# Kernel optimization log

Hardware: AMD Instinct MI355X
Metric: run time of the kernel (lower is better)

## Reference

```python
import jax, jax.numpy as jnp
import numpy as np

D_MODEL = 1024
N_HEADS = 16
D_HEAD = D_MODEL // N_HEADS
ROPE_BASE = 10000.0


def _rotate_half(x):
    half = x.shape[-1] // 2
    x1, x2 = x[..., :half], x[..., half:]
    return jnp.concatenate([-x2, x1], axis=-1)


def _rope_cos_sin(seq_len, d_head, dtype):
    inv_freq = 1.0 / (ROPE_BASE ** (jnp.arange(0, d_head, 2, dtype=jnp.float32) / d_head))
    t = jnp.arange(seq_len, dtype=jnp.float32)
    freqs = jnp.outer(t, inv_freq)                       # [S, d_head/2]
    emb = jnp.concatenate([freqs, freqs], axis=-1)       # [S, d_head]
    return jnp.cos(emb).astype(dtype), jnp.sin(emb).astype(dtype)


def setup_inputs() -> dict:
    key = jax.random.key(0)
    k1, k2, k3 = jax.random.split(key, 3)
    B, S = 2, 2048
    x = jax.random.normal(k1, (B, S, D_MODEL), dtype=jnp.float32)
    # torch nn.Linear weight layout: [out_features, in_features], y = x @ W.T
    w_qkv = jax.random.normal(k2, (3 * D_MODEL, D_MODEL), dtype=jnp.float32) * (D_MODEL ** -0.5)
    w_out = jax.random.normal(k3, (D_MODEL, D_MODEL), dtype=jnp.float32) * (D_MODEL ** -0.5)
    return {"x": x, "w_qkv": w_qkv, "w_out": w_out}


def reference(x, w_qkv, w_out):
    B, S, _ = x.shape
    qkv = jnp.einsum('bsd,ed->bse', x, w_qkv)            # [B, S, 3*D]
    qkv = qkv.reshape(B, S, 3, N_HEADS, D_HEAD)
    qkv = jnp.transpose(qkv, (2, 0, 3, 1, 4))            # [3, B, H, S, Dh]
    q, k, v = qkv[0], qkv[1], qkv[2]

    cos, sin = _rope_cos_sin(S, D_HEAD, x.dtype)         # [S, Dh] each
    cos = cos[None, None]                                # [1, 1, S, Dh]
    sin = sin[None, None]
    q = q * cos + _rotate_half(q) * sin
    k = k * cos + _rotate_half(k) * sin

    scale = 1.0 / jnp.sqrt(jnp.array(D_HEAD, dtype=x.dtype))
    attn = jnp.einsum('bhqd,bhkd->bhqk', q, k) * scale   # [B, H, S, S]
    causal = jnp.tril(jnp.ones((S, S), dtype=bool))      # triu(diag=1) masked -> keep lower tri
    attn = jnp.where(causal[None, None], attn, jnp.finfo(x.dtype).min)
    attn = jax.nn.softmax(attn, axis=-1)

    out = jnp.einsum('bhqk,bhkd->bhqd', attn, v)         # [B, H, S, Dh]
    out = jnp.transpose(out, (0, 2, 1, 3)).reshape(B, S, D_MODEL)
    return jnp.einsum('bsd,ed->bse', out, w_out)         # out_proj
```

## Files before the change

### kernel.cpp

```cpp
#include <hip/hip_runtime.h>
#include <hip/hip_bf16.h>
#include <cmath>

#define DMODEL 1024
#define NH 16
#define DH 64
#define SEQ 2048
#define BATCH 2

typedef __attribute__((ext_vector_type(8))) short bf16x8;
typedef __attribute__((ext_vector_type(4))) float f32x4;
typedef __attribute__((ext_vector_type(8))) unsigned short u16x8;

__device__ __forceinline__ unsigned short f2bf(float f) {
    unsigned int u = __builtin_bit_cast(unsigned int, f);
    u += 0x7fffu + ((u >> 16) & 1u);
    return (unsigned short)(u >> 16);
}
__device__ __forceinline__ float exp2_fast(float x) {
    float r;
    asm("v_exp_f32 %0, %1" : "=v"(r) : "v"(x));
    return r;
}

__global__ __launch_bounds__(256)
void cast_all(const float* __restrict__ x, const float* __restrict__ wq,
              const float* __restrict__ wo, unsigned short* __restrict__ xb,
              unsigned short* __restrict__ wqb, unsigned short* __restrict__ wob)
{
    const int i = blockIdx.x * 256 + threadIdx.x;
    const float* src; unsigned short* dst; int off;
    if (i < 524288)      { src = x;  dst = xb;  off = i; }
    else if (i < 917504) { src = wq; dst = wqb; off = i - 524288; }
    else                 { src = wo; dst = wob; off = i - 917504; }
    const float4 a = *(const float4*)(src + (size_t)off * 8);
    const float4 b = *(const float4*)(src + (size_t)off * 8 + 4);
    u16x8 o;
    o[0] = f2bf(a.x); o[1] = f2bf(a.y); o[2] = f2bf(a.z); o[3] = f2bf(a.w);
    o[4] = f2bf(b.x); o[5] = f2bf(b.y); o[6] = f2bf(b.z); o[7] = f2bf(b.w);
    *(u16x8*)(dst + (size_t)off * 8) = o;
}

template<int BM, int EPI>
__global__ __launch_bounds__(256)
void gemm_bf16(const unsigned short* __restrict__ A,
               const unsigned short* __restrict__ B,
               float* __restrict__ oc, unsigned short* __restrict__ oq,
               unsigned short* __restrict__ ok, unsigned short* __restrict__ ovt,
               int M, int N)
{
    constexpr int K = 1024;
    constexpr int BK = 32;
    constexpr int NT = K / BK;
    constexpr int FM = BM / 32;
    __shared__ unsigned short As[2][BM * BK];
    __shared__ unsigned short Bs[2][128 * BK];

    const int t  = threadIdx.x;
    const int l  = t & 63;
    const int w  = t >> 6;
    const int g  = l >> 4;
    const int ln = l & 15;
    const int wr = w >> 1, wc = w & 1;
    const int m0 = blockIdx.y * BM;
    const int n0 = blockIdx.x * 128;

    auto stage = [&](int kt, int bufi) {
        #pragma unroll
        for (int i = 0; i < BM / 64; ++i) {
            const int n = i * 256 + t;
            const int r = n >> 2, slot = n & 3;
            const int kk = kt * BK + ((slot ^ ((r >> 1) & 3)) * 8);
            const unsigned short* ga = A + (size_t)(m0 + r) * K + kk;
            __builtin_amdgcn_global_load_lds(
                (const __attribute__((address_space(1))) unsigned int*)ga,
                (__attribute__((address_space(3))) unsigned int*)&As[bufi][n * 8], 16, 0, 0);
        }
        #pragma unroll
        for (int i = 0; i < 2; ++i) {
            const int n = i * 256 + t;
            const int r = n >> 2, slot = n & 3;
            const int kk = kt * BK + ((slot ^ ((r >> 1) & 3)) * 8);
            const unsigned short* gb = B + (size_t)(n0 + r) * K + kk;
            __builtin_amdgcn_global_load_lds(
                (const __attribute__((address_space(1))) unsigned int*)gb,
                (__attribute__((address_space(3))) unsigned int*)&Bs[bufi][n * 8], 16, 0, 0);
        }
    };

    f32x4 acc[FM][4];
    #pragma unroll
    for (int i = 0; i < FM; ++i)
        #pragma unroll
        for (int j = 0; j < 4; ++j) acc[i][j] = (f32x4){0.f, 0.f, 0.f, 0.f};

    const int swz = (g ^ ((ln >> 1) & 3)) << 4;

    stage(0, 0);
    for (int kt = 0; kt < NT; ++kt) {
        __syncthreads();
        if (kt + 1 < NT) stage(kt + 1, (kt + 1) & 1);
        const char* as = (const char*)As[kt & 1];
        const char* bs = (const char*)Bs[kt & 1];
        bf16x8 af[FM], bfr[4];
        #pragma unroll
        for (int fm = 0; fm < FM; ++fm)
            af[fm] = *(const bf16x8*)(as + (wr * (BM / 2) + fm * 16 + ln) * 64 + swz);
        #pragma unroll
        for (int fn = 0; fn < 4; ++fn)
            bfr[fn] = *(const bf16x8*)(bs + (wc * 64 + fn * 16 + ln) * 64 + swz);
        #pragma unroll
        for (int fm = 0; fm < FM; ++fm)
            #pragma unroll
            for (int fn = 0; fn < 4; ++fn)
                acc[fm][fn] = __builtin_amdgcn_mfma_f32_16x16x32_bf16(
                    af[fm], bfr[fn], acc[fm][fn], 0, 0, 0);
    }

    const int rowbase = m0 + wr * (BM / 2);
    const int colbase = n0 + wc * 64;
    if (EPI == 1) {
        #pragma unroll
        for (int fm = 0; fm < FM; ++fm)
            #pragma unroll
            for (int fn = 0; fn < 4; ++fn)
                #pragma unroll
                for (int rr = 0; rr < 4; ++rr) {
                    const int row = rowbase + fm * 16 + g * 4 + rr;
                    oc[(size_t)row * N + colbase + fn * 16 + ln] = acc[fm][fn][rr];
                }
    } else {
        const int which = colbase >> 10;
        const int h = (colbase >> 6) & (NH - 1);
        if (which < 2) {
            unsigned short* dst = which == 0 ? oq : ok;
            const float scale = which == 0 ? 0.18033688011112042f : 1.f;
            const float cexp = -13.287712379549449f / 32.f;
            const float if0 = exp2f((float)ln * cexp);
            const float if1 = exp2f((float)(16 + ln) * cexp);
            #pragma unroll
            for (int fm = 0; fm < FM; ++fm)
                #pragma unroll
                for (int rr = 0; rr < 4; ++rr) {
                    const int row = rowbase + fm * 16 + g * 4 + rr;
                    const int b = row >> 11, s = row & (SEQ - 1);
                    float s0, c0, s1, c1;
                    __sincosf((float)s * if0, &s0, &c0);
                    __sincosf((float)s * if1, &s1, &c1);
                    const float x0 = acc[fm][0][rr], x1 = acc[fm][1][rr];
                    const float x2 = acc[fm][2][rr], x3 = acc[fm][3][rr];
                    const size_t base = (((size_t)b * NH + h) * SEQ + s) * DH;
                    dst[base + ln]      = f2bf((x0 * c0 - x2 * s0) * scale);
                    dst[base + 16 + ln] = f2bf((x1 * c1 - x3 * s1) * scale);
                    dst[base + 32 + ln] = f2bf((x2 * c0 + x0 * s0) * scale);
                    dst[base + 48 + ln] = f2bf((x3 * c1 + x1 * s1) * scale);
                }
        } else {
            #pragma unroll
            for (int fm = 0; fm < FM; ++fm)
                #pragma unroll
                for (int fn = 0; fn < 4; ++fn) {
                    const int row = rowbase + fm * 16 + g * 4;
                    const int b = row >> 11, s = row & (SEQ - 1);
                    const int d = fn * 16 + ln;
                    ushort4 pk;
                    pk.x = f2bf(acc[fm][fn][0]); pk.y = f2bf(acc[fm][fn][1]);
                    pk.z = f2bf(acc[fm][fn][2]); pk.w = f2bf(acc[fm][fn][3]);
                    *(ushort4*)&ovt[(((size_t)b * NH + h) * DH + d) * SEQ + s] = pk;
                }
        }
    }
}

__global__ __launch_bounds__(256)
void attn_mfma(const unsigned short* __restrict__ q,
               const unsigned short* __restrict__ k,
               const unsigned short* __restrict__ vt,
               unsigned short* __restrict__ ob)
{
    __shared__ unsigned short Ks[2][64 * 64];
    __shared__ unsigned short Vs[2][64 * 64];
    __shared__ unsigned short Ps[2][4][16 * 64];

    const int t  = threadIdx.x;
    const int l  = t & 63;
    const int w  = t >> 6;
    const int g  = l >> 4;
    const int ln = l & 15;
    const int pi = blockIdx.x;
    const int qtA = pi, qtB = 31 - pi;
    const int bh = blockIdx.y;
    const size_t bqk = (size_t)bh * SEQ * DH;
    const size_t bv  = (size_t)bh * DH * SEQ;

    bf16x8 qfA0, qfA1, qfB0, qfB1;
    {
        const unsigned short* qa = q + bqk + (size_t)(qtA * 64 + w * 16 + ln) * DH + g * 8;
        qfA0 = *(const bf16x8*)qa;  qfA1 = *(const bf16x8*)(qa + 32);
        const unsigned short* qb2 = q + bqk + (size_t)(qtB * 64 + w * 16 + ln) * DH + g * 8;
        qfB0 = *(const bf16x8*)qb2; qfB1 = *(const bf16x8*)(qb2 + 32);
    }

    f32x4 aoA[4], aoB[4];
    #pragma unroll
    for (int i = 0; i < 4; ++i) {
        aoA[i] = (f32x4){0.f, 0.f, 0.f, 0.f};
        aoB[i] = (f32x4){0.f, 0.f, 0.f, 0.f};
    }
    float lA = 0.f, lB = 0.f;

    auto stage = [&](int kt, int bufi) {
        #pragma unroll
        for (int rr = 0; rr < 2; ++rr) {
            const int id  = rr * 256 + t;
            const int row = id >> 3, sl = id & 7;
            const int slg = (sl ^ (row & 7)) * 8;
            const unsigned short* gk = k  + bqk + (size_t)(kt * 64 + row) * DH + slg;
            const unsigned short* gv = vt + bv  + (size_t)row * SEQ + kt * 64 + slg;
            __builtin_amdgcn_global_load_lds(
                (const __attribute__((address_space(1))) unsigned int*)gk,
                (__attribute__((address_space(3))) unsigned int*)&Ks[bufi][id * 8], 16, 0, 0);
            __builtin_amdgcn_global_load_lds(
                (const __attribute__((address_space(1))) unsigned int*)gv,
                (__attribute__((address_space(3))) unsigned int*)&Vs[bufi][id * 8], 16, 0, 0);
        }
    };

    auto softmax_tile = [&](f32x4* s, float& l_, char* pb) {
        const float M2 = 28.853900817779268f;
        float rs = 0.f;
        #pragma unroll
        for (int nb = 0; nb < 4; ++nb) {
            float e[4];
            #pragma unroll
            for (int r = 0; r < 4; ++r)
                e[r] = exp2_fast(s[nb][r] - M2);
            rs += (e[0] + e[1]) + (e[2] + e[3]);
            uint2 dw;
            dw.x = __builtin_amdgcn_perm(
                __builtin_bit_cast(unsigned int, e[1]),
                __builtin_bit_cast(unsigned int, e[0]), 0x07060302u);
            dw.y = __builtin_amdgcn_perm(
                __builtin_bit_cast(unsigned int, e[3]),
                __builtin_bit_cast(unsigned int, e[2]), 0x07060302u);
            *(uint2*)(pb + ((nb * 32 + g * 8) ^ ((ln & 7) << 4))) = dw;
        }
        rs += __shfl_xor(rs, 16);
        rs += __shfl_xor(rs, 32);
        l_ += rs;
    };

    char* pbA = (char*)&Ps[0][w][0] + ln * 128;
    char* pbB = (char*)&Ps[1][w][0] + ln * 128;

    stage(0, 0);
    for (int kt = 0; kt <= qtB; ++kt) {
        __syncthreads();
        if (kt < qtB) stage(kt + 1, (kt + 1) & 1);
        const bool actA = (kt <= qtA);
        const char* kb = (const char*)Ks[kt & 1];
        const char* vb = (const char*)Vs[kt & 1];

        f32x4 sA[4], sB[4];
        #pragma unroll
        for (int nb = 0; nb < 4; ++nb) {
            sA[nb] = (f32x4){0.f, 0.f, 0.f, 0.f};
            sB[nb] = (f32x4){0.f, 0.f, 0.f, 0.f};
        }
        __builtin_amdgcn_s_setprio(1);
        #pragma unroll
        for (int nb = 0; nb < 4; ++nb) {
            const int key = nb * 16 + ln;
            const char* kr = kb + key * 128;
            bf16x8 kf0 = *(const bf16x8*)(kr + ((g ^ (key & 7)) << 4));
            bf16x8 kf1 = *(const bf16x8*)(kr + (((g + 4) ^ (key & 7)) << 4));
            sB[nb] = __builtin_amdgcn_mfma_f32_16x16x32_bf16(kf0, qfB0, sB[nb], 0, 0, 0);
            sB[nb] = __builtin_amdgcn_mfma_f32_16x16x32_bf16(kf1, qfB1, sB[nb], 0, 0, 0);
            if (actA) {
                sA[nb] = __builtin_amdgcn_mfma_f32_16x16x32_bf16(kf0, qfA0, sA[nb], 0, 0, 0);
                sA[nb] = __builtin_amdgcn_mfma_f32_16x16x32_bf16(kf1, qfA1, sA[nb], 0, 0, 0);
            }
        }
        __builtin_amdgcn_s_setprio(0);

        if (kt == qtB) {
            #pragma unroll
            for (int nb = 0; nb < 4; ++nb)
                #pragma unroll
                for (int r = 0; r < 4; ++r)
                    if (nb * 16 + g * 4 + r > w * 16 + ln) sB[nb][r] = -INFINITY;
        }
        if (kt == qtA) {
            #pragma unroll
            for (int nb = 0; nb < 4; ++nb)
                #pragma unroll
                for (int r = 0; r < 4; ++r)
                    if (nb * 16 + g * 4 + r > w * 16 + ln) sA[nb][r] = -INFINITY;
        }

        softmax_tile(sB, lB, pbB);
        if (actA) softmax_tile(sA, lA, pbA);

        __builtin_amdgcn_s_setprio(1);
        #pragma unroll
        for (int ks = 0; ks < 2; ++ks) {
            bf16x8 pfB = *(const bf16x8*)(pbB + ((ks * 64 + g * 16) ^ ((ln & 7) << 4)));
            bf16x8 pfA;
            if (actA)
                pfA = *(const bf16x8*)(pbA + ((ks * 64 + g * 16) ^ ((ln & 7) << 4)));
            #pragma unroll
            for (int db = 0; db < 4; ++db) {
                const int d = db * 16 + ln;
                bf16x8 vf = *(const bf16x8*)(vb + d * 128 + (((ks * 4 + g) ^ (d & 7)) << 4));
                aoB[db] = __builtin_amdgcn_mfma_f32_16x16x32_bf16(pfB, vf, aoB[db], 0, 0, 0);
                if (actA)
                    aoA[db] = __builtin_amdgcn_mfma_f32_16x16x32_bf16(pfA, vf, aoA[db], 0, 0, 0);
            }
        }
        __builtin_amdgcn_s_setprio(0);
    }

    const int b = bh >> 4, h = bh & (NH - 1);
    const float invA = 1.f / lA, invB = 1.f / lB;
    #pragma unroll
    for (int r = 0; r < 4; ++r) {
        const float iA = __shfl(invA, g * 4 + r);
        const float iB = __shfl(invB, g * 4 + r);
        const size_t rowA = (size_t)(b * SEQ + qtA * 64 + w * 16 + g * 4 + r) * DMODEL + h * DH;
        const size_t rowB = (size_t)(b * SEQ + qtB * 64 + w * 16 + g * 4 + r) * DMODEL + h * DH;
        #pragma unroll
        for (int db = 0; db < 4; ++db) {
            ob[rowA + db * 16 + ln] = f2bf(aoA[db][r] * iA);
            ob[rowB + db * 16 + ln] = f2bf(aoB[db][r] * iB);
        }
    }
}

extern "C" void kernel_launch(void* const* d_in, const int* in_sizes, int n_in,
                              void* d_out, int out_size, void* d_ws, size_t ws_size,
                              hipStream_t stream)
{
    const float* x  = (const float*)d_in[0];
    const float* wq = (const float*)d_in[1];
    const float* wo = (const float*)d_in[2];
    float* out = (float*)d_out;

    const size_t NQ = (size_t)BATCH * NH * SEQ * DH;
    unsigned short* qb  = (unsigned short*)d_ws;
    unsigned short* kb  = qb + NQ;
    unsigned short* vtb = kb + NQ;
    unsigned short* ob  = vtb + NQ;
    unsigned short* xb  = ob + NQ;
    unsigned short* wqb = xb + NQ;
    unsigned short* wob = wqb + 3 * DMODEL * DMODEL;

    cast_all<<<4096, 256, 0, stream>>>(x, wq, wo, xb, wqb, wob);

    dim3 g1(3072 / 128, 4096 / 128);
    gemm_bf16<128, 0><<<g1, 256, 0, stream>>>(xb, wqb, nullptr, qb, kb, vtb, 4096, 3072);

    dim3 g2(16, BATCH * NH);
    attn_mfma<<<g2, 256, 0, stream>>>(qb, kb, vtb, ob);

    dim3 g3(1024 / 128, 4096 / 64);
    gemm_bf16<64, 1><<<g3, 256, 0, stream>>>(ob, wob, out, nullptr, nullptr, nullptr, 4096, 1024);
}
```

Baseline: 124.4 us.

## Keep softmax probabilities in registers by permuting key order in QK^T tiles

Reorders which keys each MFMA lane group computes in the QK^T step, so the output accumulator layout matches the A-operand layout needed for the PV MFMA. This lets the bf16 probabilities stay in registers instead of being written to and read back from an LDS staging buffer. The K/V LDS swizzle and causal mask indices are changed to match the new key permutation. The per-tile row-sum shuffles are moved out of the loop into a single reduction at the end. The index mapping is subtle, and any mismatch between the new swizzle and the permutation would give wrong results or LDS bank conflicts.

```diff
diff --git a/kernel.cpp b/kernel.cpp
--- a/kernel.cpp
+++ b/kernel.cpp
@@ -10,6 +10,7 @@
 
 typedef __attribute__((ext_vector_type(8))) short bf16x8;
 typedef __attribute__((ext_vector_type(4))) float f32x4;
+typedef __attribute__((ext_vector_type(4))) unsigned int u32x4;
 typedef __attribute__((ext_vector_type(8))) unsigned short u16x8;
 
 __device__ __forceinline__ unsigned short f2bf(float f) {
@@ -180,7 +181,6 @@
 {
     __shared__ unsigned short Ks[2][64 * 64];
     __shared__ unsigned short Vs[2][64 * 64];
-    __shared__ unsigned short Ps[2][4][16 * 64];
 
     const int t  = threadIdx.x;
     const int l  = t & 63;
@@ -214,7 +214,8 @@
         for (int rr = 0; rr < 2; ++rr) {
             const int id  = rr * 256 + t;
             const int row = id >> 3, sl = id & 7;
-            const int slg = (sl ^ (row & 7)) * 8;
+            const int sg  = (row & 3) | (((row >> 3) & 1) << 2);
+            const int slg = (sl ^ sg) * 8;
             const unsigned short* gk = k  + bqk + (size_t)(kt * 64 + row) * DH + slg;
             const unsigned short* gv = vt + bv  + (size_t)row * SEQ + kt * 64 + slg;
             __builtin_amdgcn_global_load_lds(
@@ -226,9 +227,16 @@
         }
     };
 
-    auto softmax_tile = [&](f32x4* s, float& l_, char* pb) {
+    const int rowoffK = ((ln >> 2) * 8 + (ln & 3)) * 128;
+    const int sK = (ln & 3) | (((ln >> 2) & 1) << 2);
+    const int slotK0 = ((g ^ sK) << 4);
+    const int slotK1 = (((g + 4) ^ sK) << 4);
+    const int sV = (ln & 3) | (((ln >> 3) & 1) << 2);
+
+    auto softmax_tile = [&](f32x4* s, float& l_, bf16x8* pf) {
         const float M2 = 28.853900817779268f;
         float rs = 0.f;
+        unsigned int dw[8];
         #pragma unroll
         for (int nb = 0; nb < 4; ++nb) {
             float e[4];
@@ -236,22 +244,17 @@
             for (int r = 0; r < 4; ++r)
                 e[r] = exp2_fast(s[nb][r] - M2);
             rs += (e[0] + e[1]) + (e[2] + e[3]);
-            uint2 dw;
-            dw.x = __builtin_amdgcn_perm(
+            dw[nb * 2] = __builtin_amdgcn_perm(
                 __builtin_bit_cast(unsigned int, e[1]),
                 __builtin_bit_cast(unsigned int, e[0]), 0x07060302u);
-            dw.y = __builtin_amdgcn_perm(
+            dw[nb * 2 + 1] = __builtin_amdgcn_perm(
                 __builtin_bit_cast(unsigned int, e[3]),
                 __builtin_bit_cast(unsigned int, e[2]), 0x07060302u);
-            *(uint2*)(pb + ((nb * 32 + g * 8) ^ ((ln & 7) << 4))) = dw;
-        }
-        rs += __shfl_xor(rs, 16);
-        rs += __shfl_xor(rs, 32);
+        }
         l_ += rs;
+        pf[0] = __builtin_bit_cast(bf16x8, (u32x4){dw[0], dw[1], dw[2], dw[3]});
+        pf[1] = __builtin_bit_cast(bf16x8, (u32x4){dw[4], dw[5], dw[6], dw[7]});
     };
-
-    char* pbA = (char*)&Ps[0][w][0] + ln * 128;
-    char* pbB = (char*)&Ps[1][w][0] + ln * 128;
 
     stage(0, 0);
     for (int kt = 0; kt <= qtB; ++kt) {
@@ -270,10 +273,9 @@
         __builtin_amdgcn_s_setprio(1);
         #pragma unroll
         for (int nb = 0; nb < 4; ++nb) {
-            const int key = nb * 16 + ln;
-            const char* kr = kb + key * 128;
-            bf16x8 kf0 = *(const bf16x8*)(kr + ((g ^ (key & 7)) << 4));
-            bf16x8 kf1 = *(const bf16x8*)(kr + (((g + 4) ^ (key & 7)) << 4));
+            const char* kr = kb + ((nb >> 1) * 32 + (nb & 1) * 4) * 128 + rowoffK;
+            bf16x8 kf0 = *(const bf16x8*)(kr + slotK0);
+            bf16x8 kf1 = *(const bf16x8*)(kr + slotK1);
             sB[nb] = __builtin_amdgcn_mfma_f32_16x16x32_bf16(kf0, qfB0, sB[nb], 0, 0, 0);
             sB[nb] = __builtin_amdgcn_mfma_f32_16x16x32_bf16(kf1, qfB1, sB[nb], 0, 0, 0);
             if (actA) {
@@ -288,38 +290,39 @@
             for (int nb = 0; nb < 4; ++nb)
                 #pragma unroll
                 for (int r = 0; r < 4; ++r)
-                    if (nb * 16 + g * 4 + r > w * 16 + ln) sB[nb][r] = -INFINITY;
+                    if ((nb >> 1) * 32 + g * 8 + (nb & 1) * 4 + r > w * 16 + ln)
+                        sB[nb][r] = -INFINITY;
         }
         if (kt == qtA) {
             #pragma unroll
             for (int nb = 0; nb < 4; ++nb)
                 #pragma unroll
                 for (int r = 0; r < 4; ++r)
-                    if (nb * 16 + g * 4 + r > w * 16 + ln) sA[nb][r] = -INFINITY;
-        }
-
-        softmax_tile(sB, lB, pbB);
-        if (actA) softmax_tile(sA, lA, pbA);
+                    if ((nb >> 1) * 32 + g * 8 + (nb & 1) * 4 + r > w * 16 + ln)
+                        sA[nb][r] = -INFINITY;
+        }
+
+        bf16x8 pfA[2], pfB[2];
+        softmax_tile(sB, lB, pfB);
+        if (actA) softmax_tile(sA, lA, pfA);
 
         __builtin_amdgcn_s_setprio(1);
         #pragma unroll
         for (int ks = 0; ks < 2; ++ks) {
-            bf16x8 pfB = *(const bf16x8*)(pbB + ((ks * 64 + g * 16) ^ ((ln & 7) << 4)));
-            bf16x8 pfA;
-            if (actA)
-                pfA = *(const bf16x8*)(pbA + ((ks * 64 + g * 16) ^ ((ln & 7) << 4)));
             #pragma unroll
             for (int db = 0; db < 4; ++db) {
                 const int d = db * 16 + ln;
-                bf16x8 vf = *(const bf16x8*)(vb + d * 128 + (((ks * 4 + g) ^ (d & 7)) << 4));
-                aoB[db] = __builtin_amdgcn_mfma_f32_16x16x32_bf16(pfB, vf, aoB[db], 0, 0, 0);
+                bf16x8 vf = *(const bf16x8*)(vb + d * 128 + (((ks * 4 + g) ^ sV) << 4));
+                aoB[db] = __builtin_amdgcn_mfma_f32_16x16x32_bf16(pfB[ks], vf, aoB[db], 0, 0, 0);
                 if (actA)
-                    aoA[db] = __builtin_amdgcn_mfma_f32_16x16x32_bf16(pfA, vf, aoA[db], 0, 0, 0);
+                    aoA[db] = __builtin_amdgcn_mfma_f32_16x16x32_bf16(pfA[ks], vf, aoA[db], 0, 0, 0);
             }
         }
         __builtin_amdgcn_s_setprio(0);
     }
 
+    lA += __shfl_xor(lA, 16); lA += __shfl_xor(lA, 32);
+    lB += __shfl_xor(lB, 16); lB += __shfl_xor(lB, 32);
     const int b = bh >> 4, h = bh & (NH - 1);
     const float invA = 1.f / lA, invB = 1.f / lB;
     #pragma unroll
```

After: 121.9 us. 1.02x faster.
